# Kernel tuning notes

Hardware: AMD Instinct MI355X
Metric: run time of the kernel (lower is better)

## Reference

```python
import jax, jax.numpy as jnp
import numpy as np

B, S, E, H = 2, 2048, 1024, 16
D = E // H  # head_dim = 64


def setup_inputs() -> dict:
    key = jax.random.key(0)
    ks = jax.random.split(key, 5)
    return {
        "hidden_states": jax.random.normal(ks[0], (B, S, E), jnp.float32),
        "c_attn_w": jax.random.normal(ks[1], (E, 3 * E), jnp.float32) * 0.02,
        "c_attn_b": jnp.zeros((3 * E,), jnp.float32),
        "c_proj_w": jax.random.normal(ks[2], (E, E), jnp.float32) * 0.02,
        "c_proj_b": jnp.zeros((E,), jnp.float32),
    }


def reference(hidden_states, c_attn_w, c_attn_b, c_proj_w, c_proj_b):
    # Conv1D: x @ w + b -> qkv [B, S, 3E]
    qkv = hidden_states @ c_attn_w + c_attn_b
    q, k, v = jnp.split(qkv, 3, axis=-1)
    # [B, H, S, D]
    q = q.reshape(B, S, H, D).transpose(0, 2, 1, 3)
    k = k.reshape(B, S, H, D).transpose(0, 2, 1, 3)
    v = v.reshape(B, S, H, D).transpose(0, 2, 1, 3)
    # scores [B, H, S, S], scaled by sqrt(head_dim)
    scores = jnp.einsum("bhqd,bhkd->bhqk", q, k) / jnp.sqrt(jnp.asarray(D, q.dtype))
    causal = jnp.tril(jnp.ones((S, S), bool))  # [S, S]
    mask_value = jnp.finfo(scores.dtype).min
    scores = jnp.where(causal, scores, mask_value)
    attn = jax.nn.softmax(scores, axis=-1)
    # attn @ V -> [B, H, S, D] -> [B, S, E]
    out = jnp.einsum("bhqk,bhkd->bhqd", attn, v)
    out = out.transpose(0, 2, 1, 3).reshape(B, S, E)
    return out @ c_proj_w + c_proj_b
```

## Files before the change

### kernel.cpp

```cpp
#include <hip/hip_runtime.h>

using bf16 = __bf16;
typedef __bf16 bf16x8 __attribute__((ext_vector_type(8)));
typedef __bf16 bf16x4 __attribute__((ext_vector_type(4)));
typedef float  f32x4  __attribute__((ext_vector_type(4)));

#define MFMA16(a, b, c) __builtin_amdgcn_mfma_f32_16x16x32_bf16((a), (b), (c), 0, 0, 0)

static constexpr int S = 2048, E = 1024;
static constexpr float CSCALE = 0.18033688011112042f;

__device__ __forceinline__ void gld16(const bf16* g, bf16* l) {
    __builtin_amdgcn_global_load_lds((const __attribute__((address_space(1))) unsigned*)g,
                                     (__attribute__((address_space(3))) unsigned*)l, 16, 0, 0);
}

__global__ __launch_bounds__(256) void k_cvt(const float* __restrict__ in, bf16* __restrict__ out, int n) {
    int i = (blockIdx.x * 256 + threadIdx.x) * 4;
    if (i >= n) return;
    float4 v = *(const float4*)(in + i);
    bf16x4 o = { (bf16)v.x, (bf16)v.y, (bf16)v.z, (bf16)v.w };
    *(bf16x4*)(out + i) = o;
}

__global__ __launch_bounds__(256) void k_tcvt(const float* __restrict__ in, bf16* __restrict__ out, int K, int N) {
    __shared__ float tile[32][33];
    int bx = blockIdx.x * 32;
    int by = blockIdx.y * 32;
    int tx = threadIdx.x & 31, ty = threadIdx.x >> 5;
#pragma unroll
    for (int i = 0; i < 32; i += 8)
        tile[ty + i][tx] = in[(long)(by + ty + i) * N + bx + tx];
    __syncthreads();
#pragma unroll
    for (int i = 0; i < 32; i += 8)
        out[(long)(bx + ty + i) * K + by + tx] = (bf16)tile[tx][ty + i];
}

template <bool OUT_F32>
__global__ __launch_bounds__(256) void k_gemm_bt(const bf16* __restrict__ A, const bf16* __restrict__ Bt,
                                                 const float* __restrict__ bias, void* __restrict__ Cout,
                                                 int Mm, int Nn, int Kk, int scale_cols, float scale) {
    const int bm = blockIdx.x * 128;
    const int bn = blockIdx.y * 128;
    const int tid = threadIdx.x;
    const int w = tid >> 6, lane = tid & 63;
    const int wm = (w >> 1) * 64, wn = (w & 1) * 64;
    const int col = lane & 15, quad = lane >> 4;

    __shared__ bf16 sA[128 * 32];
    __shared__ bf16 sB[128 * 32];

    const int c0 = w * 128 + lane;
    const int r0 = c0 >> 2, s0 = c0 & 3;
    const int r1 = (c0 + 64) >> 2, s1 = (c0 + 64) & 3;
    const bf16* pA0 = A + (long)(bm + r0) * Kk + s0 * 8;
    const bf16* pA1 = A + (long)(bm + r1) * Kk + s1 * 8;
    const bf16* pB0 = Bt + (long)(bn + r0) * Kk + s0 * 8;
    const bf16* pB1 = Bt + (long)(bn + r1) * Kk + s1 * 8;
    bf16* lA0 = sA + w * 1024;
    bf16* lA1 = sA + w * 1024 + 512;
    bf16* lB0 = sB + w * 1024;
    bf16* lB1 = sB + w * 1024 + 512;

    f32x4 acc[4][4] = {};

    for (int k0 = 0; k0 < Kk; k0 += 32) {
        __syncthreads();
        gld16(pA0 + k0, lA0);
        gld16(pA1 + k0, lA1);
        gld16(pB0 + k0, lB0);
        gld16(pB1 + k0, lB1);
        __syncthreads();
        bf16x8 af[4], bfr[4];
#pragma unroll
        for (int mt = 0; mt < 4; mt++) af[mt] = *(const bf16x8*)(sA + (wm + mt * 16 + col) * 32 + quad * 8);
#pragma unroll
        for (int nt = 0; nt < 4; nt++) bfr[nt] = *(const bf16x8*)(sB + (wn + nt * 16 + col) * 32 + quad * 8);
#pragma unroll
        for (int mt = 0; mt < 4; mt++)
#pragma unroll
            for (int nt = 0; nt < 4; nt++)
                acc[mt][nt] = MFMA16(af[mt], bfr[nt], acc[mt][nt]);
    }

#pragma unroll
    for (int mt = 0; mt < 4; mt++) {
        const int gr = bm + wm + mt * 16 + quad * 4;
#pragma unroll
        for (int nt = 0; nt < 4; nt++) {
            const int gc = bn + wn + nt * 16 + col;
            const float bv = bias[gc];
            const float sc = (gc < scale_cols) ? scale : 1.0f;
#pragma unroll
            for (int r = 0; r < 4; r++) {
                float vv = (acc[mt][nt][r] + bv) * sc;
                if (OUT_F32) ((float*)Cout)[(long)(gr + r) * Nn + gc] = vv;
                else         ((bf16*)Cout)[(long)(gr + r) * Nn + gc] = (bf16)vv;
            }
        }
    }
}

__global__ __launch_bounds__(256) void k_gemm_bt64(const bf16* __restrict__ A, const bf16* __restrict__ Bt,
                                                    const float* __restrict__ bias, float* __restrict__ Cout,
                                                    int Mm, int Nn, int Kk) {
    const int bm = blockIdx.x * 64;
    const int bn = blockIdx.y * 128;
    const int tid = threadIdx.x;
    const int w = tid >> 6, lane = tid & 63;
    const int wm = (w >> 1) * 32, wn = (w & 1) * 64;
    const int col = lane & 15, quad = lane >> 4;

    __shared__ bf16 sA[64 * 32];
    __shared__ bf16 sB[128 * 32];

    const int ca = w * 64 + lane;
    const int ra = ca >> 2, sa = ca & 3;
    const int c0 = w * 128 + lane;
    const int r0 = c0 >> 2, s0 = c0 & 3;
    const int r1 = (c0 + 64) >> 2, s1 = (c0 + 64) & 3;
    const bf16* pA0 = A + (long)(bm + ra) * Kk + sa * 8;
    const bf16* pB0 = Bt + (long)(bn + r0) * Kk + s0 * 8;
    const bf16* pB1 = Bt + (long)(bn + r1) * Kk + s1 * 8;
    bf16* lA0 = sA + w * 512;
    bf16* lB0 = sB + w * 1024;
    bf16* lB1 = sB + w * 1024 + 512;

    f32x4 acc[2][4] = {};

    for (int k0 = 0; k0 < Kk; k0 += 32) {
        __syncthreads();
        gld16(pA0 + k0, lA0);
        gld16(pB0 + k0, lB0);
        gld16(pB1 + k0, lB1);
        __syncthreads();
        bf16x8 af[2], bfr[4];
#pragma unroll
        for (int mt = 0; mt < 2; mt++) af[mt] = *(const bf16x8*)(sA + (wm + mt * 16 + col) * 32 + quad * 8);
#pragma unroll
        for (int nt = 0; nt < 4; nt++) bfr[nt] = *(const bf16x8*)(sB + (wn + nt * 16 + col) * 32 + quad * 8);
#pragma unroll
        for (int mt = 0; mt < 2; mt++)
#pragma unroll
            for (int nt = 0; nt < 4; nt++)
                acc[mt][nt] = MFMA16(af[mt], bfr[nt], acc[mt][nt]);
    }

#pragma unroll
    for (int mt = 0; mt < 2; mt++) {
        const int gr = bm + wm + mt * 16 + quad * 4;
#pragma unroll
        for (int nt = 0; nt < 4; nt++) {
            const int gc = bn + wn + nt * 16 + col;
            const float bv = bias[gc];
#pragma unroll
            for (int r = 0; r < 4; r++)
                Cout[(long)(gr + r) * Nn + gc] = acc[mt][nt][r] + bv;
        }
    }
}

__global__ __launch_bounds__(256) void k_attn(const bf16* __restrict__ qkv, bf16* __restrict__ out) {
    const int p = blockIdx.x;
    const int bh = blockIdx.y;
    const int b = bh >> 4, h = bh & 15;
    const int tid = threadIdx.x;
    const int w = tid >> 6, lane = tid & 63;
    const int col = lane & 15, quad = lane >> 4;

    __shared__ bf16 sK[2][64 * 72];
    __shared__ bf16 sVt[2][64 * 80];
    __shared__ bf16 sP[4][16 * 72];

    const long base = (long)b * S * 3072;
    const int ko = E + h * 64, vo = 2 * E + h * 64;

    const int krow = tid >> 2, kcol = (tid & 3) * 16;
    const int vkk = (tid & 31) * 2, vd0 = (tid >> 5) * 4;
    const bf16* kgp = qkv + base + (long)krow * 3072 + ko + kcol;
    const bf16* vgp = qkv + base + (long)vkk * 3072 + vo + vd0;
    bf16* pw = sP[w];

    bf16x8 kr0 = *(const bf16x8*)(kgp);
    bf16x8 kr1 = *(const bf16x8*)(kgp + 8);
    ushort4 va0 = *(const ushort4*)(vgp);
    ushort4 vb0 = *(const ushort4*)(vgp + 3072);
    ushort4 va1 = *(const ushort4*)(vgp + 32);
    ushort4 vb1 = *(const ushort4*)(vgp + 3072 + 32);

    int buf = 0;
#pragma unroll 1
    for (int sel = 0; sel < 2; sel++) {
        const int qt = sel ? p : 31 - p;
        const int q0 = qt * 64;
        bf16x8 bq0, bq1;
        {
            const bf16* qp = qkv + base + (long)(q0 + w * 16 + col) * 3072 + h * 64 + quad * 8;
            bq0 = *(const bf16x8*)(qp);
            bq1 = *(const bf16x8*)(qp + 32);
        }
        float m_ = -1e30f, l_ = 0.f;
        f32x4 o0 = {}, o1 = {}, o2 = {}, o3 = {};

#pragma unroll 1
        for (int kt = 0; kt <= qt; kt++) {
            bf16* bK = sK[buf];
            bf16* bV = sVt[buf];
            buf ^= 1;
            *(bf16x8*)(bK + krow * 72 + kcol) = kr0;
            *(bf16x8*)(bK + krow * 72 + kcol + 8) = kr1;
            *(unsigned*)(bV + (vd0 + 0) * 80 + vkk) = (unsigned)va0.x | ((unsigned)vb0.x << 16);
            *(unsigned*)(bV + (vd0 + 1) * 80 + vkk) = (unsigned)va0.y | ((unsigned)vb0.y << 16);
            *(unsigned*)(bV + (vd0 + 2) * 80 + vkk) = (unsigned)va0.z | ((unsigned)vb0.z << 16);
            *(unsigned*)(bV + (vd0 + 3) * 80 + vkk) = (unsigned)va0.w | ((unsigned)vb0.w << 16);
            *(unsigned*)(bV + (vd0 + 32) * 80 + vkk) = (unsigned)va1.x | ((unsigned)vb1.x << 16);
            *(unsigned*)(bV + (vd0 + 33) * 80 + vkk) = (unsigned)va1.y | ((unsigned)vb1.y << 16);
            *(unsigned*)(bV + (vd0 + 34) * 80 + vkk) = (unsigned)va1.z | ((unsigned)vb1.z << 16);
            *(unsigned*)(bV + (vd0 + 35) * 80 + vkk) = (unsigned)va1.w | ((unsigned)vb1.w << 16);
            __syncthreads();

            bool pf = true;
            long noff = 0;
            if (kt < qt) noff = (long)(kt + 1) * 64 * 3072;
            else if (sel == 1) pf = false;
            if (pf) {
                kr0 = *(const bf16x8*)(kgp + noff);
                kr1 = *(const bf16x8*)(kgp + noff + 8);
                va0 = *(const ushort4*)(vgp + noff);
                vb0 = *(const ushort4*)(vgp + noff + 3072);
                va1 = *(const ushort4*)(vgp + noff + 32);
                vb1 = *(const ushort4*)(vgp + noff + 3072 + 32);
            }

            f32x4 s[4];
#pragma unroll
            for (int mt = 0; mt < 4; mt++) {
                const bf16* kp = bK + (mt * 16 + col) * 72 + quad * 8;
                f32x4 z = {};
                z = MFMA16(*(const bf16x8*)(kp), bq0, z);
                z = MFMA16(*(const bf16x8*)(kp + 32), bq1, z);
                s[mt] = z;
            }
            if (kt == qt) {
#pragma unroll
                for (int mt = 0; mt < 4; mt++) {
                    if (mt >= w) {
#pragma unroll
                        for (int r = 0; r < 4; r++)
                            if (mt * 16 + quad * 4 + r > w * 16 + col) s[mt][r] = -1e30f;
                    }
                }
            }
            float cm = -1e30f;
#pragma unroll
            for (int mt = 0; mt < 4; mt++)
#pragma unroll
                for (int r = 0; r < 4; r++) cm = fmaxf(cm, s[mt][r]);
            cm = fmaxf(cm, __shfl_xor(cm, 16));
            cm = fmaxf(cm, __shfl_xor(cm, 32));
            const float mnew = fmaxf(m_, cm);
            const float alpha = __builtin_amdgcn_exp2f(m_ - mnew);
            m_ = mnew;
            float rs = 0.f;
#pragma unroll
            for (int mt = 0; mt < 4; mt++)
#pragma unroll
                for (int r = 0; r < 4; r++) {
                    float pe = __builtin_amdgcn_exp2f(s[mt][r] - mnew);
                    s[mt][r] = pe;
                    rs += pe;
                }
            l_ = l_ * alpha + rs;
#pragma unroll
            for (int r = 0; r < 4; r++) { o0[r] *= alpha; o1[r] *= alpha; o2[r] *= alpha; o3[r] *= alpha; }
#pragma unroll
            for (int mt = 0; mt < 4; mt++) {
                bf16x4 pk = { (bf16)s[mt][0], (bf16)s[mt][1], (bf16)s[mt][2], (bf16)s[mt][3] };
                *(bf16x4*)(pw + col * 72 + mt * 16 + quad * 4) = pk;
            }
#pragma unroll
            for (int ks = 0; ks < 2; ks++) {
                bf16x8 ap = *(const bf16x8*)(pw + col * 72 + ks * 32 + quad * 8);
                const bf16* vb = bV + col * 80 + ks * 32 + quad * 8;
                o0 = MFMA16(*(const bf16x8*)(vb),           ap, o0);
                o1 = MFMA16(*(const bf16x8*)(vb + 16 * 80), ap, o1);
                o2 = MFMA16(*(const bf16x8*)(vb + 32 * 80), ap, o2);
                o3 = MFMA16(*(const bf16x8*)(vb + 48 * 80), ap, o3);
            }
        }

        float lt = l_;
        lt += __shfl_xor(lt, 16);
        lt += __shfl_xor(lt, 32);
        const float li = 1.f / lt;
        bf16* op = out + (long)(b * S + q0 + w * 16 + col) * E + h * 64 + quad * 4;
        f32x4 oo[4] = { o0, o1, o2, o3 };
#pragma unroll
        for (int mt = 0; mt < 4; mt++) {
            bf16x4 ov = { (bf16)(oo[mt][0] * li), (bf16)(oo[mt][1] * li),
                          (bf16)(oo[mt][2] * li), (bf16)(oo[mt][3] * li) };
            *(bf16x4*)(op + mt * 16) = ov;
        }
    }
}

extern "C" void kernel_launch(void* const* d_in, const int* in_sizes, int n_in,
                              void* d_out, int out_size, void* d_ws, size_t ws_size,
                              hipStream_t stream) {
    const float* hs = (const float*)d_in[0];
    const float* w0 = (const float*)d_in[1];
    const float* b0 = (const float*)d_in[2];
    const float* w1 = (const float*)d_in[3];
    const float* b1 = (const float*)d_in[4];
    float* outp = (float*)d_out;

    char* ws = (char*)d_ws;
    bf16* A0   = (bf16*)(ws);
    bf16* Wt0  = (bf16*)(ws + 8388608);
    bf16* Wt1  = (bf16*)(ws + 14680064);
    bf16* qkv  = (bf16*)(ws + 16777216);
    bf16* attn = (bf16*)(ws + 41943040);

    k_cvt<<<4096, 256, 0, stream>>>(hs, A0, 4194304);
    k_tcvt<<<dim3(96, 32), 256, 0, stream>>>(w0, Wt0, 1024, 3072);
    k_tcvt<<<dim3(32, 32), 256, 0, stream>>>(w1, Wt1, 1024, 1024);
    k_gemm_bt<false><<<dim3(32, 24), 256, 0, stream>>>(A0, Wt0, b0, qkv, 4096, 3072, 1024, 1024, CSCALE);
    k_attn<<<dim3(16, 32), 256, 0, stream>>>(qkv, attn);
    k_gemm_bt64<<<dim3(64, 8), 256, 0, stream>>>(attn, Wt1, b1, outp, 4096, 1024, 1024);
}
```

Measured before the change: 203.4 us.

## Widen attention query tile to 128 rows and merge prep kernels

New measurement: 187.2 us. 8.0% less time.

```diff
diff --git a/kernel.cpp b/kernel.cpp
--- a/kernel.cpp
+++ b/kernel.cpp
@@ -15,26 +15,35 @@
                                      (__attribute__((address_space(3))) unsigned*)l, 16, 0, 0);
 }
 
-__global__ __launch_bounds__(256) void k_cvt(const float* __restrict__ in, bf16* __restrict__ out, int n) {
-    int i = (blockIdx.x * 256 + threadIdx.x) * 4;
-    if (i >= n) return;
-    float4 v = *(const float4*)(in + i);
-    bf16x4 o = { (bf16)v.x, (bf16)v.y, (bf16)v.z, (bf16)v.w };
-    *(bf16x4*)(out + i) = o;
-}
-
-__global__ __launch_bounds__(256) void k_tcvt(const float* __restrict__ in, bf16* __restrict__ out, int K, int N) {
+__global__ __launch_bounds__(256) void k_prep(const float* __restrict__ hs, const float* __restrict__ w0,
+                                              const float* __restrict__ w1, bf16* __restrict__ A0,
+                                              bf16* __restrict__ Wt0, bf16* __restrict__ Wt1) {
     __shared__ float tile[32][33];
-    int bx = blockIdx.x * 32;
-    int by = blockIdx.y * 32;
-    int tx = threadIdx.x & 31, ty = threadIdx.x >> 5;
+    const int bx = blockIdx.x;
+    if (bx < 4096) {
+        int i = (bx * 256 + threadIdx.x) * 4;
+        float4 v = *(const float4*)(hs + i);
+        bf16x4 o = { (bf16)v.x, (bf16)v.y, (bf16)v.z, (bf16)v.w };
+        *(bf16x4*)(A0 + i) = o;
+        return;
+    }
+    const float* in;
+    bf16* outp;
+    int K, N, nb, kb;
+    if (bx < 4096 + 3072) {
+        int j = bx - 4096; in = w0; outp = Wt0; K = 1024; N = 3072; nb = j % 96; kb = j / 96;
+    } else {
+        int j = bx - 7168; in = w1; outp = Wt1; K = 1024; N = 1024; nb = j % 32; kb = j / 32;
+    }
+    const int bxx = nb * 32, byy = kb * 32;
+    const int tx = threadIdx.x & 31, ty = threadIdx.x >> 5;
 #pragma unroll
     for (int i = 0; i < 32; i += 8)
-        tile[ty + i][tx] = in[(long)(by + ty + i) * N + bx + tx];
+        tile[ty + i][tx] = in[(long)(byy + ty + i) * N + bxx + tx];
     __syncthreads();
 #pragma unroll
     for (int i = 0; i < 32; i += 8)
-        out[(long)(bx + ty + i) * K + by + tx] = (bf16)tile[tx][ty + i];
+        outp[(long)(bxx + ty + i) * K + byy + tx] = (bf16)tile[tx][ty + i];
 }
 
 template <bool OUT_F32>
@@ -162,19 +171,31 @@
 }
 
 __global__ __launch_bounds__(256) void k_attn(const bf16* __restrict__ qkv, bf16* __restrict__ out) {
-    const int p = blockIdx.x;
-    const int bh = blockIdx.y;
+    const int L = blockIdx.x;
+    const int bh = L & 31;
+    const int t = L >> 5;
+    const int qt = (t < 8) ? (15 - t) : (t - 8);
     const int b = bh >> 4, h = bh & 15;
     const int tid = threadIdx.x;
     const int w = tid >> 6, lane = tid & 63;
     const int col = lane & 15, quad = lane >> 4;
+    const int q0 = qt * 128;
+    const int nkt = 2 * qt + 2;
 
     __shared__ bf16 sK[2][64 * 72];
     __shared__ bf16 sVt[2][64 * 80];
-    __shared__ bf16 sP[4][16 * 72];
+    __shared__ bf16 sP[4][32 * 72];
 
     const long base = (long)b * S * 3072;
     const int ko = E + h * 64, vo = 2 * E + h * 64;
+
+    bf16x8 bq[2][2];
+#pragma unroll
+    for (int qg = 0; qg < 2; qg++) {
+        const bf16* qp = qkv + base + (long)(q0 + w * 32 + qg * 16 + col) * 3072 + h * 64 + quad * 8;
+        bq[qg][0] = *(const bf16x8*)(qp);
+        bq[qg][1] = *(const bf16x8*)(qp + 32);
+    }
 
     const int krow = tid >> 2, kcol = (tid & 3) * 16;
     const int vkk = (tid & 31) * 2, vd0 = (tid >> 5) * 4;
@@ -189,118 +210,123 @@
     ushort4 va1 = *(const ushort4*)(vgp + 32);
     ushort4 vb1 = *(const ushort4*)(vgp + 3072 + 32);
 
+    float m_[2] = { -1e30f, -1e30f }, l_[2] = { 0.f, 0.f };
+    f32x4 o[2][4] = {};
+
     int buf = 0;
 #pragma unroll 1
-    for (int sel = 0; sel < 2; sel++) {
-        const int qt = sel ? p : 31 - p;
-        const int q0 = qt * 64;
-        bf16x8 bq0, bq1;
-        {
-            const bf16* qp = qkv + base + (long)(q0 + w * 16 + col) * 3072 + h * 64 + quad * 8;
-            bq0 = *(const bf16x8*)(qp);
-            bq1 = *(const bf16x8*)(qp + 32);
-        }
-        float m_ = -1e30f, l_ = 0.f;
-        f32x4 o0 = {}, o1 = {}, o2 = {}, o3 = {};
-
-#pragma unroll 1
-        for (int kt = 0; kt <= qt; kt++) {
-            bf16* bK = sK[buf];
-            bf16* bV = sVt[buf];
-            buf ^= 1;
-            *(bf16x8*)(bK + krow * 72 + kcol) = kr0;
-            *(bf16x8*)(bK + krow * 72 + kcol + 8) = kr1;
-            *(unsigned*)(bV + (vd0 + 0) * 80 + vkk) = (unsigned)va0.x | ((unsigned)vb0.x << 16);
-            *(unsigned*)(bV + (vd0 + 1) * 80 + vkk) = (unsigned)va0.y | ((unsigned)vb0.y << 16);
-            *(unsigned*)(bV + (vd0 + 2) * 80 + vkk) = (unsigned)va0.z | ((unsigned)vb0.z << 16);
-            *(unsigned*)(bV + (vd0 + 3) * 80 + vkk) = (unsigned)va0.w | ((unsigned)vb0.w << 16);
-            *(unsigned*)(bV + (vd0 + 32) * 80 + vkk) = (unsigned)va1.x | ((unsigned)vb1.x << 16);
-            *(unsigned*)(bV + (vd0 + 33) * 80 + vkk) = (unsigned)va1.y | ((unsigned)vb1.y << 16);
-            *(unsigned*)(bV + (vd0 + 34) * 80 + vkk) = (unsigned)va1.z | ((unsigned)vb1.z << 16);
-            *(unsigned*)(bV + (vd0 + 35) * 80 + vkk) = (unsigned)va1.w | ((unsigned)vb1.w << 16);
-            __syncthreads();
-
-            bool pf = true;
-            long noff = 0;
-            if (kt < qt) noff = (long)(kt + 1) * 64 * 3072;
-            else if (sel == 1) pf = false;
-            if (pf) {
-                kr0 = *(const bf16x8*)(kgp + noff);
-                kr1 = *(const bf16x8*)(kgp + noff + 8);
-                va0 = *(const ushort4*)(vgp + noff);
-                vb0 = *(const ushort4*)(vgp + noff + 3072);
-                va1 = *(const ushort4*)(vgp + noff + 32);
-                vb1 = *(const ushort4*)(vgp + noff + 3072 + 32);
-            }
-
-            f32x4 s[4];
-#pragma unroll
-            for (int mt = 0; mt < 4; mt++) {
-                const bf16* kp = bK + (mt * 16 + col) * 72 + quad * 8;
+    for (int kt = 0; kt < nkt; kt++) {
+        bf16* bK = sK[buf];
+        bf16* bV = sVt[buf];
+        buf ^= 1;
+        *(bf16x8*)(bK + krow * 72 + kcol) = kr0;
+        *(bf16x8*)(bK + krow * 72 + kcol + 8) = kr1;
+        *(unsigned*)(bV + (vd0 + 0) * 80 + vkk) = (unsigned)va0.x | ((unsigned)vb0.x << 16);
+        *(unsigned*)(bV + (vd0 + 1) * 80 + vkk) = (unsigned)va0.y | ((unsigned)vb0.y << 16);
+        *(unsigned*)(bV + (vd0 + 2) * 80 + vkk) = (unsigned)va0.z | ((unsigned)vb0.z << 16);
+        *(unsigned*)(bV + (vd0 + 3) * 80 + vkk) = (unsigned)va0.w | ((unsigned)vb0.w << 16);
+        *(unsigned*)(bV + (vd0 + 32) * 80 + vkk) = (unsigned)va1.x | ((unsigned)vb1.x << 16);
+        *(unsigned*)(bV + (vd0 + 33) * 80 + vkk) = (unsigned)va1.y | ((unsigned)vb1.y << 16);
+        *(unsigned*)(bV + (vd0 + 34) * 80 + vkk) = (unsigned)va1.z | ((unsigned)vb1.z << 16);
+        *(unsigned*)(bV + (vd0 + 35) * 80 + vkk) = (unsigned)va1.w | ((unsigned)vb1.w << 16);
+        __syncthreads();
+
+        if (kt + 1 < nkt) {
+            const long noff = (long)(kt + 1) * 64 * 3072;
+            kr0 = *(const bf16x8*)(kgp + noff);
+            kr1 = *(const bf16x8*)(kgp + noff + 8);
+            va0 = *(const ushort4*)(vgp + noff);
+            vb0 = *(const ushort4*)(vgp + noff + 3072);
+            va1 = *(const ushort4*)(vgp + noff + 32);
+            vb1 = *(const ushort4*)(vgp + noff + 3072 + 32);
+        }
+
+        f32x4 s[2][4];
+#pragma unroll
+        for (int mt = 0; mt < 4; mt++) {
+            const bf16* kp = bK + (mt * 16 + col) * 72 + quad * 8;
+            const bf16x8 ka0 = *(const bf16x8*)(kp);
+            const bf16x8 ka1 = *(const bf16x8*)(kp + 32);
+#pragma unroll
+            for (int qg = 0; qg < 2; qg++) {
                 f32x4 z = {};
-                z = MFMA16(*(const bf16x8*)(kp), bq0, z);
-                z = MFMA16(*(const bf16x8*)(kp + 32), bq1, z);
-                s[mt] = z;
-            }
-            if (kt == qt) {
-#pragma unroll
-                for (int mt = 0; mt < 4; mt++) {
-                    if (mt >= w) {
-#pragma unroll
-                        for (int r = 0; r < 4; r++)
-                            if (mt * 16 + quad * 4 + r > w * 16 + col) s[mt][r] = -1e30f;
-                    }
-                }
-            }
+                z = MFMA16(ka0, bq[qg][0], z);
+                z = MFMA16(ka1, bq[qg][1], z);
+                s[qg][mt] = z;
+            }
+        }
+        if (kt >= 2 * qt) {
+#pragma unroll
+            for (int qg = 0; qg < 2; qg++) {
+                const int qrow = q0 + w * 32 + qg * 16 + col;
+#pragma unroll
+                for (int mt = 0; mt < 4; mt++)
+#pragma unroll
+                    for (int r = 0; r < 4; r++)
+                        if (kt * 64 + mt * 16 + quad * 4 + r > qrow) s[qg][mt][r] = -1e30f;
+            }
+        }
+#pragma unroll
+        for (int qg = 0; qg < 2; qg++) {
             float cm = -1e30f;
 #pragma unroll
             for (int mt = 0; mt < 4; mt++)
 #pragma unroll
-                for (int r = 0; r < 4; r++) cm = fmaxf(cm, s[mt][r]);
+                for (int r = 0; r < 4; r++) cm = fmaxf(cm, s[qg][mt][r]);
             cm = fmaxf(cm, __shfl_xor(cm, 16));
             cm = fmaxf(cm, __shfl_xor(cm, 32));
-            const float mnew = fmaxf(m_, cm);
-            const float alpha = __builtin_amdgcn_exp2f(m_ - mnew);
-            m_ = mnew;
+            const float mnew = fmaxf(m_[qg], cm);
+            const float alpha = __builtin_amdgcn_exp2f(m_[qg] - mnew);
+            m_[qg] = mnew;
             float rs = 0.f;
 #pragma unroll
             for (int mt = 0; mt < 4; mt++)
 #pragma unroll
                 for (int r = 0; r < 4; r++) {
-                    float pe = __builtin_amdgcn_exp2f(s[mt][r] - mnew);
-                    s[mt][r] = pe;
+                    float pe = __builtin_amdgcn_exp2f(s[qg][mt][r] - mnew);
+                    s[qg][mt][r] = pe;
                     rs += pe;
                 }
-            l_ = l_ * alpha + rs;
-#pragma unroll
-            for (int r = 0; r < 4; r++) { o0[r] *= alpha; o1[r] *= alpha; o2[r] *= alpha; o3[r] *= alpha; }
+            l_[qg] = l_[qg] * alpha + rs;
+#pragma unroll
+            for (int dt = 0; dt < 4; dt++)
+#pragma unroll
+                for (int r = 0; r < 4; r++) o[qg][dt][r] *= alpha;
 #pragma unroll
             for (int mt = 0; mt < 4; mt++) {
-                bf16x4 pk = { (bf16)s[mt][0], (bf16)s[mt][1], (bf16)s[mt][2], (bf16)s[mt][3] };
-                *(bf16x4*)(pw + col * 72 + mt * 16 + quad * 4) = pk;
-            }
-#pragma unroll
-            for (int ks = 0; ks < 2; ks++) {
-                bf16x8 ap = *(const bf16x8*)(pw + col * 72 + ks * 32 + quad * 8);
-                const bf16* vb = bV + col * 80 + ks * 32 + quad * 8;
-                o0 = MFMA16(*(const bf16x8*)(vb),           ap, o0);
-                o1 = MFMA16(*(const bf16x8*)(vb + 16 * 80), ap, o1);
-                o2 = MFMA16(*(const bf16x8*)(vb + 32 * 80), ap, o2);
-                o3 = MFMA16(*(const bf16x8*)(vb + 48 * 80), ap, o3);
-            }
-        }
-
-        float lt = l_;
+                bf16x4 pk = { (bf16)s[qg][mt][0], (bf16)s[qg][mt][1],
+                              (bf16)s[qg][mt][2], (bf16)s[qg][mt][3] };
+                *(bf16x4*)(pw + (qg * 16 + col) * 72 + mt * 16 + quad * 4) = pk;
+            }
+        }
+#pragma unroll
+        for (int ks = 0; ks < 2; ks++) {
+            bf16x8 vf[4];
+#pragma unroll
+            for (int dt = 0; dt < 4; dt++)
+                vf[dt] = *(const bf16x8*)(bV + (dt * 16 + col) * 80 + ks * 32 + quad * 8);
+#pragma unroll
+            for (int qg = 0; qg < 2; qg++) {
+                bf16x8 ap = *(const bf16x8*)(pw + (qg * 16 + col) * 72 + ks * 32 + quad * 8);
+#pragma unroll
+                for (int dt = 0; dt < 4; dt++)
+                    o[qg][dt] = MFMA16(vf[dt], ap, o[qg][dt]);
+            }
+        }
+    }
+
+#pragma unroll
+    for (int qg = 0; qg < 2; qg++) {
+        float lt = l_[qg];
         lt += __shfl_xor(lt, 16);
         lt += __shfl_xor(lt, 32);
         const float li = 1.f / lt;
-        bf16* op = out + (long)(b * S + q0 + w * 16 + col) * E + h * 64 + quad * 4;
-        f32x4 oo[4] = { o0, o1, o2, o3 };
-#pragma unroll
-        for (int mt = 0; mt < 4; mt++) {
-            bf16x4 ov = { (bf16)(oo[mt][0] * li), (bf16)(oo[mt][1] * li),
-                          (bf16)(oo[mt][2] * li), (bf16)(oo[mt][3] * li) };
-            *(bf16x4*)(op + mt * 16) = ov;
+        bf16* op = out + (long)(b * S + q0 + w * 32 + qg * 16 + col) * E + h * 64 + quad * 4;
+#pragma unroll
+        for (int dt = 0; dt < 4; dt++) {
+            bf16x4 ov = { (bf16)(o[qg][dt][0] * li), (bf16)(o[qg][dt][1] * li),
+                          (bf16)(o[qg][dt][2] * li), (bf16)(o[qg][dt][3] * li) };
+            *(bf16x4*)(op + dt * 16) = ov;
         }
     }
 }
@@ -322,10 +348,8 @@
     bf16* qkv  = (bf16*)(ws + 16777216);
     bf16* attn = (bf16*)(ws + 41943040);
 
-    k_cvt<<<4096, 256, 0, stream>>>(hs, A0, 4194304);
-    k_tcvt<<<dim3(96, 32), 256, 0, stream>>>(w0, Wt0, 1024, 3072);
-    k_tcvt<<<dim3(32, 32), 256, 0, stream>>>(w1, Wt1, 1024, 1024);
+    k_prep<<<8192, 256, 0, stream>>>(hs, w0, w1, A0, Wt0, Wt1);
     k_gemm_bt<false><<<dim3(32, 24), 256, 0, stream>>>(A0, Wt0, b0, qkv, 4096, 3072, 1024, 1024, CSCALE);
-    k_attn<<<dim3(16, 32), 256, 0, stream>>>(qkv, attn);
+    k_attn<<<512, 256, 0, stream>>>(qkv, attn);
     k_gemm_bt64<<<dim3(64, 8), 256, 0, stream>>>(attn, Wt1, b1, outp, 4096, 1024, 1024);
 }
```
